# Performance work log

Hardware: AMD Instinct MI355X
Metric: run time of the kernel (lower is better)

## Reference

```python
import jax, jax.numpy as jnp
import numpy as np

B = 16384          # batch
F = 26             # num sparse features
D = 13             # num dense features
V = 100000         # vocab per sparse feature
E = 16             # embedding size
HID = [400, 400, 400]
DNN_IN = F * E + D  # 429


def setup_inputs() -> dict:
    key = jax.random.key(0)
    ks = jax.random.split(key, 16)
    inp = {}
    inp["x_sparse"] = jax.random.randint(ks[0], (B, F), 0, V, dtype=jnp.int32)
    inp["x_dense"] = jax.random.uniform(ks[1], (B, D), dtype=jnp.float32)
    # embedding tables (stacked across features; all vocabs equal)
    inp["emb1"] = jax.random.normal(ks[2], (F, V, 1), dtype=jnp.float32) * 0.0001
    inp["emb2"] = jax.random.normal(ks[3], (F, V, E), dtype=jnp.float32) * 0.0001
    inp["w_dense"] = jax.random.normal(ks[4], (D, 1), dtype=jnp.float32) * 0.0001
    inp["bias"] = jnp.zeros((1,), dtype=jnp.float32)
    dims = [DNN_IN] + HID
    for i in range(3):
        inp[f"dnn_w{i}"] = jax.random.normal(ks[5 + i], (dims[i], dims[i + 1]), dtype=jnp.float32) * 0.02
        inp[f"dnn_b{i}"] = jnp.zeros((dims[i + 1],), dtype=jnp.float32)
    inp["final_w"] = jax.random.normal(ks[9], (HID[-1], 1), dtype=jnp.float32) * 0.02
    return inp


def reference(x_sparse, x_dense, emb1, emb2, w_dense, bias,
              dnn_w0, dnn_b0, dnn_w1, dnn_b1, dnn_w2, dnn_b2, final_w):
    f_idx = jnp.arange(F)[None, :]                      # [1, F]
    # FM linear: per-feature 1-d embedding lookup, summed over features
    e1 = emb1[f_idx, x_sparse, 0]                       # [B, F]
    linear_sparse = jnp.sum(e1, axis=-1, keepdims=True)  # [B, 1]
    linear_dense = x_dense @ w_dense                    # [B, 1]
    logit = linear_sparse + linear_dense
    # FM second order: square-of-sum minus sum-of-square
    fm = emb2[f_idx, x_sparse]                          # [B, F, E]
    s = jnp.sum(fm, axis=1)                             # [B, E]
    cross = 0.5 * jnp.sum(s * s - jnp.sum(fm * fm, axis=1), axis=-1, keepdims=True)  # [B, 1]
    logit = logit + cross
    # DNN
    h = jnp.concatenate([fm.reshape(x_sparse.shape[0], F * E), x_dense], axis=-1)  # [B, F*E+D]
    h = jax.nn.relu(h @ dnn_w0 + dnn_b0)
    h = jax.nn.relu(h @ dnn_w1 + dnn_b1)
    h = jax.nn.relu(h @ dnn_w2 + dnn_b2)
    logit = logit + h @ final_w                         # [B, 1]
    return jax.nn.sigmoid(logit + bias)
```

## Files before the change

### kernel.cpp

```cpp
#include <hip/hip_runtime.h>
#include <hip/hip_bf16.h>
#include <math.h>

#define BATCH 16384
#define NF 26
#define ND 13
#define VOC 100000
#define KP0 448
#define KP1 416
#define CS 80
#define NSL 5
#define NBP 2080

typedef __bf16 bf16x8 __attribute__((ext_vector_type(8)));
typedef float f32x4 __attribute__((ext_vector_type(4)));
using bf16 = __hip_bfloat16;
typedef unsigned short u16;

__device__ __forceinline__ void gload_lds16(const void* g, void* l) {
  __builtin_amdgcn_global_load_lds(
      (const __attribute__((address_space(1))) void*)g,
      (__attribute__((address_space(3))) void*)l, 16, 0, 0);
}

__device__ __forceinline__ u16 f2bu(float v) {
  union { __hip_bfloat16 b; u16 u; } cv;
  cv.b = __float2bfloat16(v);
  return cv.u;
}

__global__ __launch_bounds__(256) void prep_gather_kernel(
    const float* __restrict__ w0, const float* __restrict__ w1,
    const float* __restrict__ w2, bf16* __restrict__ wt0,
    bf16* __restrict__ wt1, bf16* __restrict__ wt2,
    const int* __restrict__ xs, const float* __restrict__ xd,
    const float* __restrict__ emb1, const float* __restrict__ emb2,
    const float* __restrict__ wd, const float* __restrict__ biasp,
    bf16* __restrict__ h0, float* __restrict__ partial) {
  const int bid = blockIdx.x, tid = threadIdx.x;
  if (bid < NBP) {
    const float* W; bf16* Wt; int K, KP, idx;
    if (bid < 728)       { W = w0; Wt = wt0; K = 429; KP = KP0; idx = bid * 256 + tid; }
    else if (bid < 1404) { W = w1; Wt = wt1; K = 400; KP = KP1; idx = (bid - 728) * 256 + tid; }
    else                 { W = w2; Wt = wt2; K = 400; KP = KP1; idx = (bid - 1404) * 256 + tid; }
    int k = idx % KP, n = idx / KP;
    float v = (k < K && n < 400) ? W[(size_t)k * 400 + n] : 0.f;
    Wt[idx] = __float2bfloat16(v);
    return;
  }
  const int p = bid - NBP;
  const int w = tid >> 6, lane = tid & 63;
  const int b = p * 4 + w;
  const int q = lane >> 2, sub = lane & 3;

  int xsl = 0;
  if (lane < NF) xsl = xs[b * NF + lane];
  float lin = 0.f;
  if (lane < NF) lin = emb1[(size_t)lane * VOC + xsl];
  if (lane < ND) lin += xd[b * ND + lane] * wd[lane];

  float4 sv = make_float4(0.f, 0.f, 0.f, 0.f);
  float sq = 0.f;
#pragma unroll
  for (int i = 0; i < 2; ++i) {
    int f = i * 16 + q;
    if (f < NF) {
      int idx = __shfl(xsl, f);
      float4 v = *((const float4*)(emb2 + ((size_t)f * VOC + idx) * 16) + sub);
      sv.x += v.x; sv.y += v.y; sv.z += v.z; sv.w += v.w;
      sq += v.x * v.x + v.y * v.y + v.z * v.z + v.w * v.w;
      ushort4 st;
      st.x = f2bu(v.x); st.y = f2bu(v.y); st.z = f2bu(v.z); st.w = f2bu(v.w);
      *(ushort4*)(h0 + (size_t)b * KP0 + f * 16 + sub * 4) = st;
    }
  }
  if (lane < 32) {
    float v = (lane < ND) ? xd[b * ND + lane] : 0.f;
    h0[(size_t)b * KP0 + 416 + lane] = __float2bfloat16(v);
  }
#pragma unroll
  for (int off = 4; off < 64; off <<= 1) {
    sv.x += __shfl_xor(sv.x, off);
    sv.y += __shfl_xor(sv.y, off);
    sv.z += __shfl_xor(sv.z, off);
    sv.w += __shfl_xor(sv.w, off);
  }
  float t = sv.x * sv.x + sv.y * sv.y + sv.z * sv.z + sv.w * sv.w;
#pragma unroll
  for (int off = 1; off < 64; off <<= 1) {
    t += __shfl_xor(t, off);
    sq += __shfl_xor(sq, off);
    lin += __shfl_xor(lin, off);
  }
  if (lane == 0)
    partial[b] = biasp[0] + lin + 0.5f * (t * 0.0625f - sq);
}

template <int NK, bool FINAL>
__global__ __launch_bounds__(256, 2) void gemm_kernel(
    const bf16* __restrict__ A, const bf16* __restrict__ Wt,
    const float* __restrict__ bias, bf16* __restrict__ outH,
    const float* __restrict__ fw, float* __restrict__ dotb) {
  constexpr int KP = NK * 32;
  extern __shared__ __align__(16) char smem[];
  const int b = blockIdx.x, tid = threadIdx.x;
  const int w = tid >> 6, lane = tid & 63, r = lane & 15, g = lane >> 4;
  const int lane8 = b & 7, hi = b >> 3;
  const int s = hi % NSL, mchunk = (hi / NSL) * 8 + lane8;
  const int row0 = mchunk * 128, col0 = s * CS;

  {
    const char* wbase = (const char*)(Wt + (size_t)col0 * KP);
    constexpr int T = NK * CS * 4;
    constexpr int FULL = T >> 8, REM = T & 255;
    for (int rd = 0; rd <= FULL; ++rd) {
      if (rd < FULL || tid < REM) {
        int c = rd * 256 + tid;
        int kk = c / (CS * 4), rm = c - kk * (CS * 4);
        int n = rm >> 2, j = rm & 3;
        int kc = j ^ ((n >> 1) & 3);
        gload_lds16(wbase + (size_t)n * (KP * 2) + kk * 64 + kc * 16,
                    smem + (rd * 256 + w * 64) * 16);
      }
    }
  }
  __syncthreads();

  const char* Ab = (const char*)(A + (size_t)(row0 + w * 32 + r) * KP) + g * 16;
  const size_t rtS = (size_t)16 * KP * 2;

  f32x4 acc[2][NSL];
#pragma unroll
  for (int rt = 0; rt < 2; ++rt)
#pragma unroll
    for (int ct = 0; ct < NSL; ++ct) acc[rt][ct] = (f32x4){0.f, 0.f, 0.f, 0.f};

  const int swz = ((g ^ ((r >> 1) & 3)) << 4);
  for (int k = 0; k < NK; ++k) {
    bf16x8 a0 = *(const bf16x8*)(Ab + k * 64);
    bf16x8 a1 = *(const bf16x8*)(Ab + k * 64 + rtS);
    const char* sb = smem + k * (CS * 64) + r * 64 + swz;
#pragma unroll
    for (int ct = 0; ct < NSL; ++ct) {
      bf16x8 bfr = *(const bf16x8*)(sb + ct * 1024);
      acc[0][ct] = __builtin_amdgcn_mfma_f32_16x16x32_bf16(a0, bfr, acc[0][ct], 0, 0, 0);
      acc[1][ct] = __builtin_amdgcn_mfma_f32_16x16x32_bf16(a1, bfr, acc[1][ct], 0, 0, 0);
    }
  }

  if (!FINAL) {
#pragma unroll
    for (int ct = 0; ct < NSL; ++ct) {
      int col = col0 + ct * 16 + r;
      float bv = bias[col];
#pragma unroll
      for (int rt = 0; rt < 2; ++rt)
#pragma unroll
        for (int q = 0; q < 4; ++q) {
          float v = fmaxf(acc[rt][ct][q] + bv, 0.f);
          outH[(size_t)(row0 + w * 32 + rt * 16 + g * 4 + q) * KP1 + col] =
              __float2bfloat16(v);
        }
    }
  } else {
    float pr[2][4] = {{0.f, 0.f, 0.f, 0.f}, {0.f, 0.f, 0.f, 0.f}};
#pragma unroll
    for (int ct = 0; ct < NSL; ++ct) {
      int col = col0 + ct * 16 + r;
      float bv = bias[col], fv = fw[col];
#pragma unroll
      for (int rt = 0; rt < 2; ++rt)
#pragma unroll
        for (int q = 0; q < 4; ++q)
          pr[rt][q] += fmaxf(acc[rt][ct][q] + bv, 0.f) * fv;
    }
#pragma unroll
    for (int rt = 0; rt < 2; ++rt)
#pragma unroll
      for (int q = 0; q < 4; ++q) {
        pr[rt][q] += __shfl_xor(pr[rt][q], 1);
        pr[rt][q] += __shfl_xor(pr[rt][q], 2);
        pr[rt][q] += __shfl_xor(pr[rt][q], 4);
        pr[rt][q] += __shfl_xor(pr[rt][q], 8);
      }
    if (r < 4) {
#pragma unroll
      for (int rt = 0; rt < 2; ++rt) {
        float v = (r == 0) ? pr[rt][0] : (r == 1) ? pr[rt][1]
                : (r == 2) ? pr[rt][2] : pr[rt][3];
        dotb[(size_t)s * BATCH + row0 + w * 32 + rt * 16 + g * 4 + r] = v;
      }
    }
  }
}

__global__ void finish_kernel(const float* __restrict__ partial,
                              const float* __restrict__ dotb,
                              float* __restrict__ out) {
  int i = blockIdx.x * 256 + threadIdx.x;
  if (i < BATCH) {
    float x = partial[i] + dotb[i] + dotb[BATCH + i] + dotb[2 * BATCH + i]
            + dotb[3 * BATCH + i] + dotb[4 * BATCH + i];
    out[i] = 1.f / (1.f + expf(-x));
  }
}

extern "C" void kernel_launch(void* const* d_in, const int* in_sizes, int n_in,
                              void* d_out, int out_size, void* d_ws, size_t ws_size,
                              hipStream_t stream) {
  const int* xs = (const int*)d_in[0];
  const float* xd = (const float*)d_in[1];
  const float* emb1 = (const float*)d_in[2];
  const float* emb2 = (const float*)d_in[3];
  const float* wd = (const float*)d_in[4];
  const float* bias = (const float*)d_in[5];
  const float* w0 = (const float*)d_in[6];
  const float* b0 = (const float*)d_in[7];
  const float* w1 = (const float*)d_in[8];
  const float* b1 = (const float*)d_in[9];
  const float* w2 = (const float*)d_in[10];
  const float* b2 = (const float*)d_in[11];
  const float* fw = (const float*)d_in[12];
  float* out = (float*)d_out;

  char* ws = (char*)d_ws;
  float* partial = (float*)(ws + 0);
  float* dotb    = (float*)(ws + 65536);
  bf16* wt0 = (bf16*)(ws + 393216);
  bf16* wt1 = (bf16*)(ws + 765952);
  bf16* wt2 = (bf16*)(ws + 1112064);
  bf16* h0  = (bf16*)(ws + 1458176);
  bf16* h1  = (bf16*)(ws + 16138240);
  bf16* h2  = (bf16*)(ws + 29769728);

  constexpr int LDS14 = 14 * CS * 64;
  constexpr int LDS13 = 13 * CS * 64;
  hipFuncSetAttribute((const void*)gemm_kernel<14, false>,
                      hipFuncAttributeMaxDynamicSharedMemorySize, LDS14);
  hipFuncSetAttribute((const void*)gemm_kernel<13, false>,
                      hipFuncAttributeMaxDynamicSharedMemorySize, LDS13);
  hipFuncSetAttribute((const void*)gemm_kernel<13, true>,
                      hipFuncAttributeMaxDynamicSharedMemorySize, LDS13);

  prep_gather_kernel<<<NBP + BATCH / 4, 256, 0, stream>>>(
      w0, w1, w2, wt0, wt1, wt2, xs, xd, emb1, emb2, wd, bias, h0, partial);

  gemm_kernel<14, false><<<640, 256, LDS14, stream>>>(h0, wt0, b0, h1, nullptr, nullptr);
  gemm_kernel<13, false><<<640, 256, LDS13, stream>>>(h1, wt1, b1, h2, nullptr, nullptr);
  gemm_kernel<13, true><<<640, 256, LDS13, stream>>>(h2, wt2, b2, nullptr, fw, dotb);

  finish_kernel<<<64, 256, 0, stream>>>(partial, dotb, out);
}
```

Measured before the change: 74.73 us.

## Fuse last DNN layer with final dot and sigmoid into one kernel

Replaces the third layer GEMM, which wrote per-slice partial dots to global memory, and the separate finish kernel with one kernel. Each block computes all 400 output columns for 64 rows and reduces the final-weight dot in shared memory before applying the sigmoid. This removes one launch and the dotb round trip through global memory. In exchange the new kernel reads B fragments straight from global memory without LDS staging and holds 26 accumulators per wave, which raises register pressure and may lower occupancy.

```diff
diff --git a/kernel.cpp b/kernel.cpp
--- a/kernel.cpp
+++ b/kernel.cpp
@@ -96,11 +96,10 @@
     partial[b] = biasp[0] + lin + 0.5f * (t * 0.0625f - sq);
 }
 
-template <int NK, bool FINAL>
+template <int NK>
 __global__ __launch_bounds__(256, 2) void gemm_kernel(
     const bf16* __restrict__ A, const bf16* __restrict__ Wt,
-    const float* __restrict__ bias, bf16* __restrict__ outH,
-    const float* __restrict__ fw, float* __restrict__ dotb) {
+    const float* __restrict__ bias, bf16* __restrict__ outH) {
   constexpr int KP = NK * 32;
   extern __shared__ __align__(16) char smem[];
   const int b = blockIdx.x, tid = threadIdx.x;
@@ -148,25 +147,60 @@
     }
   }
 
-  if (!FINAL) {
-#pragma unroll
-    for (int ct = 0; ct < NSL; ++ct) {
-      int col = col0 + ct * 16 + r;
-      float bv = bias[col];
-#pragma unroll
-      for (int rt = 0; rt < 2; ++rt)
-#pragma unroll
-        for (int q = 0; q < 4; ++q) {
-          float v = fmaxf(acc[rt][ct][q] + bv, 0.f);
-          outH[(size_t)(row0 + w * 32 + rt * 16 + g * 4 + q) * KP1 + col] =
-              __float2bfloat16(v);
-        }
-    }
-  } else {
-    float pr[2][4] = {{0.f, 0.f, 0.f, 0.f}, {0.f, 0.f, 0.f, 0.f}};
-#pragma unroll
-    for (int ct = 0; ct < NSL; ++ct) {
-      int col = col0 + ct * 16 + r;
+#pragma unroll
+  for (int ct = 0; ct < NSL; ++ct) {
+    int col = col0 + ct * 16 + r;
+    float bv = bias[col];
+#pragma unroll
+    for (int rt = 0; rt < 2; ++rt)
+#pragma unroll
+      for (int q = 0; q < 4; ++q) {
+        float v = fmaxf(acc[rt][ct][q] + bv, 0.f);
+        outH[(size_t)(row0 + w * 32 + rt * 16 + g * 4 + q) * KP1 + col] =
+            __float2bfloat16(v);
+      }
+  }
+}
+
+__global__ __launch_bounds__(256) void fin2_kernel(
+    const bf16* __restrict__ A, const bf16* __restrict__ Wt,
+    const float* __restrict__ bias, const float* __restrict__ fw,
+    const float* __restrict__ partial, float* __restrict__ out) {
+  __shared__ float dr[2][64];
+  const int bid = blockIdx.x, tid = threadIdx.x;
+  const int w = tid >> 6, lane = tid & 63, r = lane & 15, g = lane >> 4;
+  const int rg = w >> 1, cgp = w & 1;
+  const int ntc = cgp ? 12 : 13;
+  const int row0 = bid * 64;
+
+  const char* Ab = (const char*)(A + (size_t)(row0 + rg * 32 + r) * KP1) + g * 16;
+  const size_t rtS = (size_t)16 * KP1 * 2;
+  const char* Bb = (const char*)Wt + ((size_t)(cgp * 13 * 16 + r) * KP1) * 2 + g * 16;
+  const size_t ctS = (size_t)16 * KP1 * 2;
+
+  f32x4 acc[2][13];
+#pragma unroll
+  for (int rt = 0; rt < 2; ++rt)
+#pragma unroll
+    for (int ct = 0; ct < 13; ++ct) acc[rt][ct] = (f32x4){0.f, 0.f, 0.f, 0.f};
+
+  for (int k = 0; k < 13; ++k) {
+    bf16x8 a0 = *(const bf16x8*)(Ab + k * 64);
+    bf16x8 a1 = *(const bf16x8*)(Ab + k * 64 + rtS);
+#pragma unroll
+    for (int ct = 0; ct < 13; ++ct)
+      if (ct < ntc) {
+        bf16x8 bfr = *(const bf16x8*)(Bb + (size_t)ct * ctS + k * 64);
+        acc[0][ct] = __builtin_amdgcn_mfma_f32_16x16x32_bf16(a0, bfr, acc[0][ct], 0, 0, 0);
+        acc[1][ct] = __builtin_amdgcn_mfma_f32_16x16x32_bf16(a1, bfr, acc[1][ct], 0, 0, 0);
+      }
+  }
+
+  float pr[2][4] = {{0.f, 0.f, 0.f, 0.f}, {0.f, 0.f, 0.f, 0.f}};
+#pragma unroll
+  for (int ct = 0; ct < 13; ++ct)
+    if (ct < ntc) {
+      int col = (cgp * 13 + ct) * 16 + r;
       float bv = bias[col], fv = fw[col];
 #pragma unroll
       for (int rt = 0; rt < 2; ++rt)
@@ -175,33 +209,26 @@
           pr[rt][q] += fmaxf(acc[rt][ct][q] + bv, 0.f) * fv;
     }
 #pragma unroll
-    for (int rt = 0; rt < 2; ++rt)
-#pragma unroll
-      for (int q = 0; q < 4; ++q) {
-        pr[rt][q] += __shfl_xor(pr[rt][q], 1);
-        pr[rt][q] += __shfl_xor(pr[rt][q], 2);
-        pr[rt][q] += __shfl_xor(pr[rt][q], 4);
-        pr[rt][q] += __shfl_xor(pr[rt][q], 8);
-      }
-    if (r < 4) {
-#pragma unroll
-      for (int rt = 0; rt < 2; ++rt) {
-        float v = (r == 0) ? pr[rt][0] : (r == 1) ? pr[rt][1]
-                : (r == 2) ? pr[rt][2] : pr[rt][3];
-        dotb[(size_t)s * BATCH + row0 + w * 32 + rt * 16 + g * 4 + r] = v;
-      }
-    }
-  }
-}
-
-__global__ void finish_kernel(const float* __restrict__ partial,
-                              const float* __restrict__ dotb,
-                              float* __restrict__ out) {
-  int i = blockIdx.x * 256 + threadIdx.x;
-  if (i < BATCH) {
-    float x = partial[i] + dotb[i] + dotb[BATCH + i] + dotb[2 * BATCH + i]
-            + dotb[3 * BATCH + i] + dotb[4 * BATCH + i];
-    out[i] = 1.f / (1.f + expf(-x));
+  for (int rt = 0; rt < 2; ++rt)
+#pragma unroll
+    for (int q = 0; q < 4; ++q) {
+      pr[rt][q] += __shfl_xor(pr[rt][q], 1);
+      pr[rt][q] += __shfl_xor(pr[rt][q], 2);
+      pr[rt][q] += __shfl_xor(pr[rt][q], 4);
+      pr[rt][q] += __shfl_xor(pr[rt][q], 8);
+    }
+  if (r < 4) {
+#pragma unroll
+    for (int rt = 0; rt < 2; ++rt) {
+      float v = (r == 0) ? pr[rt][0] : (r == 1) ? pr[rt][1]
+              : (r == 2) ? pr[rt][2] : pr[rt][3];
+      dr[cgp][rg * 32 + rt * 16 + g * 4 + r] = v;
+    }
+  }
+  __syncthreads();
+  if (tid < 64) {
+    float x = partial[row0 + tid] + dr[0][tid] + dr[1][tid];
+    out[row0 + tid] = 1.f / (1.f + expf(-x));
   }
 }
 
@@ -225,7 +252,6 @@
 
   char* ws = (char*)d_ws;
   float* partial = (float*)(ws + 0);
-  float* dotb    = (float*)(ws + 65536);
   bf16* wt0 = (bf16*)(ws + 393216);
   bf16* wt1 = (bf16*)(ws + 765952);
   bf16* wt2 = (bf16*)(ws + 1112064);
@@ -235,19 +261,15 @@
 
   constexpr int LDS14 = 14 * CS * 64;
   constexpr int LDS13 = 13 * CS * 64;
-  hipFuncSetAttribute((const void*)gemm_kernel<14, false>,
+  hipFuncSetAttribute((const void*)gemm_kernel<14>,
                       hipFuncAttributeMaxDynamicSharedMemorySize, LDS14);
-  hipFuncSetAttribute((const void*)gemm_kernel<13, false>,
-                      hipFuncAttributeMaxDynamicSharedMemorySize, LDS13);
-  hipFuncSetAttribute((const void*)gemm_kernel<13, true>,
+  hipFuncSetAttribute((const void*)gemm_kernel<13>,
                       hipFuncAttributeMaxDynamicSharedMemorySize, LDS13);
 
   prep_gather_kernel<<<NBP + BATCH / 4, 256, 0, stream>>>(
       w0, w1, w2, wt0, wt1, wt2, xs, xd, emb1, emb2, wd, bias, h0, partial);
 
-  gemm_kernel<14, false><<<640, 256, LDS14, stream>>>(h0, wt0, b0, h1, nullptr, nullptr);
-  gemm_kernel<13, false><<<640, 256, LDS13, stream>>>(h1, wt1, b1, h2, nullptr, nullptr);
-  gemm_kernel<13, true><<<640, 256, LDS13, stream>>>(h2, wt2, b2, nullptr, fw, dotb);
-
-  finish_kernel<<<64, 256, 0, stream>>>(partial, dotb, out);
-}
+  gemm_kernel<14><<<640, 256, LDS14, stream>>>(h0, wt0, b0, h1);
+  gemm_kernel<13><<<640, 256, LDS13, stream>>>(h1, wt1, b1, h2);
+  fin2_kernel<<<BATCH / 64, 256, 0, stream>>>(h2, wt2, b2, fw, partial, out);
+}
```

Result: slower. 79.62 us (+6.5%).
